# Kernel optimization log

Hardware: AMD Instinct MI355X
Metric: run time of the kernel (lower is better)

The kernel has to match this reference:

```python
import jax, jax.numpy as jnp
import numpy as np

K = 16
OP_LO, OP_HI = 0.05, 0.95
SC_LO, SC_HI = 0.01, 0.5
HIDDEN = 64
B, N_IN = 32, 8192
SAMPLE_RATIO = 0.1
JITTER_STD = 0.01
DENSITY_RADIUS = 0.1
EPS = 1e-6


def _naive_fps(points, m):
    # iterative farthest-point sampling, deterministic start at index 0
    Bb, Nn, _ = points.shape
    idx0 = jnp.zeros((Bb, m), jnp.int32)
    mind0 = jnp.full((Bb, Nn), 1e10, points.dtype)

    def body(i, carry):
        idx, mind = carry
        last = jnp.take_along_axis(points, idx[:, i - 1][:, None, None], axis=1)  # [B,1,3]
        d = jnp.sum((points - last) ** 2, axis=-1)  # [B,N]
        mind = jnp.minimum(mind, d)
        nxt = jnp.argmax(mind, axis=1).astype(jnp.int32)
        idx = idx.at[:, i].set(nxt)
        return idx, mind

    idx, _ = jax.lax.fori_loop(1, m, body, (idx0, mind0))
    return idx


def _axis_angle_to_R(aa):
    angle = jnp.linalg.norm(aa, axis=-1, keepdims=True)  # [B,N,1]
    axis = aa / (angle + EPS)
    x, y, z = axis[..., 0], axis[..., 1], axis[..., 2]
    a = angle[..., 0]
    ca, sa = jnp.cos(a), jnp.sin(a)
    C = 1.0 - ca
    row0 = jnp.stack([ca + x * x * C, x * y * C - z * sa, x * z * C + y * sa], axis=-1)
    row1 = jnp.stack([y * x * C + z * sa, ca + y * y * C, y * z * C - x * sa], axis=-1)
    row2 = jnp.stack([z * x * C - y * sa, z * y * C + x * sa, ca + z * z * C], axis=-1)
    return jnp.stack([row0, row1, row2], axis=-2)  # [B,N,3,3]


def _minmax_norm(v):
    lo = v.min(axis=1, keepdims=True)
    hi = v.max(axis=1, keepdims=True)
    return (v - lo) / (hi - lo + EPS)


def _forward(points, rw1, rb1, rw2, rb2, sw1, sb1, sw2, sb2):
    pts = points.astype(jnp.float32)
    Bb, Nn, _ = pts.shape
    m = int(Nn * SAMPLE_RATIO)
    idx = _naive_fps(jax.lax.stop_gradient(pts), m)
    sampled = jnp.take_along_axis(pts, jnp.broadcast_to(idx[:, :, None], (Bb, m, 3)), axis=1)
    noise = jax.random.normal(jax.random.key(42), sampled.shape, sampled.dtype) * JITTER_STD
    pts = jnp.concatenate([sampled, sampled + noise], axis=1)  # [B, 2m, 3]

    # kNN via squared distances (same ordering as torch.cdist euclidean)
    sq = jnp.sum(pts * pts, axis=-1)
    d2 = sq[:, :, None] + sq[:, None, :] - 2.0 * jnp.einsum('bnd,bmd->bnm', pts, pts)
    _, nn = jax.lax.top_k(-d2, K + 1)
    knn = nn[:, :, 1:]  # drop self, [B,N,K]
    neighbors = jax.vmap(lambda p, i: p[i])(pts, knn)  # [B,N,K,3]

    weighted_center = neighbors.mean(axis=2)  # [B,N,3]
    # rotation head: Linear -> GELU -> Linear
    h = jax.nn.gelu(weighted_center @ rw1 + rb1, approximate=False)
    axis_angle = h @ rw2 + rb2
    angle = jnp.linalg.norm(axis_angle, axis=-1, keepdims=True)
    too_small = angle < 1e-4
    safe_angle = jnp.where(too_small, 0.0, jnp.minimum(angle, 3.14))
    default_axis = jnp.array([1.0, 0.0, 0.0], jnp.float32)
    safe_axis = jnp.where(too_small, default_axis, axis_angle / (angle + EPS))
    R = _axis_angle_to_R(safe_axis * safe_angle)

    # scale head: Linear -> GELU -> Linear -> Softplus -> Hardtanh
    hs = jax.nn.gelu(pts @ sw1 + sb1, approximate=False)
    scale = jnp.clip(jax.nn.softplus(hs @ sw2 + sb2), SC_LO, SC_HI)

    # cov = R @ diag(scale^2) @ R^T
    cov = jnp.einsum('bnij,bnj,bnkj->bnik', R, scale * scale, R)

    # opacity from neighborhood covariance spectrum + local density
    centered = neighbors - pts[:, :, None, :]  # [B,N,K,3]
    ncov = jnp.einsum('bnki,bnkj->bnij', centered, centered) / (K - 1 + EPS)
    s = jnp.linalg.svd(ncov, compute_uv=False)  # descending singular values [B,N,3]
    linearness = s[..., 0] / (s[..., 1] + s[..., 2] + EPS)
    dist2 = jnp.sum(centered * centered, axis=-1)
    density = jnp.mean((dist2 < DENSITY_RADIUS ** 2).astype(jnp.float32), axis=2)
    combined = _minmax_norm(linearness) * _minmax_norm(density) ** 0.45
    opacity = jnp.clip(combined, OP_LO, OP_HI)

    return pts, cov, opacity, R, scale


def setup_inputs() -> dict:
    key = jax.random.key(0)
    ks = jax.random.split(key, 9)

    def lin(k, fan_in, shape):
        b = 1.0 / np.sqrt(fan_in)
        return jax.random.uniform(k, shape, jnp.float32, -b, b)

    return {
        'points': jax.random.normal(ks[0], (B, N_IN, 3), jnp.float32),
        'rw1': lin(ks[1], 3, (3, HIDDEN)), 'rb1': lin(ks[2], 3, (HIDDEN,)),
        'rw2': lin(ks[3], HIDDEN, (HIDDEN, 3)), 'rb2': lin(ks[4], HIDDEN, (3,)),
        'sw1': lin(ks[5], 3, (3, HIDDEN)), 'sb1': lin(ks[6], 3, (HIDDEN,)),
        'sw2': lin(ks[7], HIDDEN, (HIDDEN, 3)), 'sb2': lin(ks[8], HIDDEN, (3,)),
    }


def reference(points, rw1, rb1, rw2, rb2, sw1, sb1, sw2, sb2):
    return _forward(points, rw1, rb1, rw2, rb2, sw1, sb1, sw2, sb2)
```

## Files before the change

kernel.cpp:

```cpp
#include <hip/hip_runtime.h>
#include <math.h>

#define BB 32
#define N_IN 8192
#define M 819
#define M2 1638
#define KNN 16
#define RPB 64
#define NCH 4
#define CHLEN 410

__device__ __forceinline__ unsigned tf_rotl(unsigned x, int r){ return (x<<r)|(x>>(32-r)); }

__device__ __forceinline__ float erfinv_xla_f32(float x){
  float w = -log1pf(-__fmul_rn(x,x));
  float p;
  if (w < 5.0f) {
    w = __fsub_rn(w, 2.5f);
    p = 2.81022636e-08f;
    p = fmaf(p, w, 3.43273939e-07f);
    p = fmaf(p, w, -3.5233877e-06f);
    p = fmaf(p, w, -4.39150654e-06f);
    p = fmaf(p, w, 0.00021858087f);
    p = fmaf(p, w, -0.00125372503f);
    p = fmaf(p, w, -0.00417768164f);
    p = fmaf(p, w, 0.246640727f);
    p = fmaf(p, w, 1.50140941f);
  } else {
    w = __fsub_rn(sqrtf(w), 3.0f);
    p = -0.000200214257f;
    p = fmaf(p, w, 0.000100950558f);
    p = fmaf(p, w, 0.00134934322f);
    p = fmaf(p, w, -0.00367342844f);
    p = fmaf(p, w, 0.00573950773f);
    p = fmaf(p, w, -0.0076224613f);
    p = fmaf(p, w, 0.00943887047f);
    p = fmaf(p, w, 1.00167406f);
    p = fmaf(p, w, 2.83297682f);
  }
  return __fmul_rn(p, x);
}

__device__ __forceinline__ float noise_at(unsigned e){
  unsigned x0 = 0u, x1 = e;
  const unsigned k0 = 0u, k1 = 42u, k2 = 0u ^ 42u ^ 0x1BD11BDAu;
  x0 += k0; x1 += k1;
#define TFR(r) { x0 += x1; x1 = tf_rotl(x1, r); x1 ^= x0; }
  TFR(13) TFR(15) TFR(26) TFR(6)   x0 += k1; x1 += k2 + 1u;
  TFR(17) TFR(29) TFR(16) TFR(24)  x0 += k2; x1 += k0 + 2u;
  TFR(13) TFR(15) TFR(26) TFR(6)   x0 += k0; x1 += k1 + 3u;
  TFR(17) TFR(29) TFR(16) TFR(24)  x0 += k1; x1 += k2 + 4u;
  TFR(13) TFR(15) TFR(26) TFR(6)   x0 += k2; x1 += k0 + 5u;
#undef TFR
  unsigned bits = x0 ^ x1;
  float f = __uint_as_float((bits >> 9) | 0x3f800000u) - 1.0f;
  const float lo = -0.99999994f;
  float u = fmaf(f, 2.0f, lo);
  u = fmaxf(lo, u);
  float z = erfinv_xla_f32(u);
  float nrm = __fmul_rn(__uint_as_float(0x3FB504F3u), z);
  return __fmul_rn(nrm, 0.01f);
}

__device__ __forceinline__ unsigned long long dpp_max_u64(unsigned long long k, const int ctrl){
  int lo = (int)(unsigned)(k & 0xffffffffull);
  int hi = (int)(unsigned)(k >> 32);
  int slo, shi;
  switch (ctrl) {
    case 0x111: slo = __builtin_amdgcn_update_dpp(lo, lo, 0x111, 0xF, 0xF, false);
                shi = __builtin_amdgcn_update_dpp(hi, hi, 0x111, 0xF, 0xF, false); break;
    case 0x112: slo = __builtin_amdgcn_update_dpp(lo, lo, 0x112, 0xF, 0xF, false);
                shi = __builtin_amdgcn_update_dpp(hi, hi, 0x112, 0xF, 0xF, false); break;
    case 0x114: slo = __builtin_amdgcn_update_dpp(lo, lo, 0x114, 0xF, 0xF, false);
                shi = __builtin_amdgcn_update_dpp(hi, hi, 0x114, 0xF, 0xF, false); break;
    case 0x118: slo = __builtin_amdgcn_update_dpp(lo, lo, 0x118, 0xF, 0xF, false);
                shi = __builtin_amdgcn_update_dpp(hi, hi, 0x118, 0xF, 0xF, false); break;
    case 0x142: slo = __builtin_amdgcn_update_dpp(lo, lo, 0x142, 0xF, 0xF, false);
                shi = __builtin_amdgcn_update_dpp(hi, hi, 0x142, 0xF, 0xF, false); break;
    default:    slo = __builtin_amdgcn_update_dpp(lo, lo, 0x143, 0xF, 0xF, false);
                shi = __builtin_amdgcn_update_dpp(hi, hi, 0x143, 0xF, 0xF, false); break;
  }
  unsigned long long o = ((unsigned long long)(unsigned)shi << 32) | (unsigned)slo;
  return (o > k) ? o : k;
}

__global__ __launch_bounds__(256, 1) void fps_kernel(const float* __restrict__ pin,
                                                     float* __restrict__ ptsO){
  const int b = blockIdx.x;
  const int t = threadIdx.x;
  const float* P = pin + (size_t)b * N_IN * 3;

  __shared__ float s_x[N_IN], s_y[N_IN], s_z[N_IN];
  __shared__ int   s_sel[M];
  __shared__ unsigned s_klo[2][4], s_khi[2][4];

  for (int i = t; i < N_IN; i += 256) {
    s_x[i] = P[i*3+0]; s_y[i] = P[i*3+1]; s_z[i] = P[i*3+2];
  }
  float px[32], py[32], pz[32], mind[32];
#pragma unroll
  for (int k = 0; k < 32; ++k) {
    int p = t + (k<<8);
    px[k] = P[p*3+0]; py[k] = P[p*3+1]; pz[k] = P[p*3+2];
    mind[k] = 1e10f;
  }
  if (t == 0) s_sel[0] = 0;
  float lx = P[0], ly = P[1], lz = P[2];
  __syncthreads();

  for (int i = 1; i < M; ++i) {
    float bv = -1.0f; int bi = 0x7fffffff;
#pragma unroll
    for (int k = 0; k < 32; ++k) {
      float dx = __fsub_rn(px[k], lx);
      float dy = __fsub_rn(py[k], ly);
      float dz = __fsub_rn(pz[k], lz);
      float d  = __fadd_rn(__fadd_rn(__fmul_rn(dx,dx), __fmul_rn(dy,dy)), __fmul_rn(dz,dz));
      float m  = fminf(mind[k], d);
      mind[k] = m;
      int idx  = t + (k<<8);
      if (m > bv) { bv = m; bi = idx; }
    }
    unsigned long long key = ((unsigned long long)__float_as_uint(bv) << 32) | (unsigned)(~bi);
    key = dpp_max_u64(key, 0x111);
    key = dpp_max_u64(key, 0x112);
    key = dpp_max_u64(key, 0x114);
    key = dpp_max_u64(key, 0x118);
    key = dpp_max_u64(key, 0x142);
    key = dpp_max_u64(key, 0x143);
    unsigned klo = (unsigned)__builtin_amdgcn_readlane((int)(unsigned)(key & 0xffffffffull), 63);
    unsigned khi = (unsigned)__builtin_amdgcn_readlane((int)(unsigned)(key >> 32), 63);
    int par = i & 1;
    if ((t & 63) == 0) { s_klo[par][t>>6] = klo; s_khi[par][t>>6] = khi; }
    __syncthreads();
    unsigned long long kb = ((unsigned long long)s_khi[par][0] << 32) | s_klo[par][0];
#pragma unroll
    for (int w2 = 1; w2 < 4; ++w2) {
      unsigned long long ko = ((unsigned long long)s_khi[par][w2] << 32) | s_klo[par][w2];
      if (ko > kb) kb = ko;
    }
    int bsel = (int)(~(unsigned)(kb & 0xffffffffull));
    if (t == 0) s_sel[i] = bsel;
    lx = s_x[bsel]; ly = s_y[bsel]; lz = s_z[bsel];
  }
  __syncthreads();

  for (int j = t; j < M; j += 256) {
    int sj = s_sel[j];
    float x = s_x[sj], y = s_y[sj], z = s_z[sj];
    float* o0 = ptsO + ((size_t)b*M2 + j)*3;
    float* o1 = o0 + (size_t)M*3;
    o0[0]=x; o0[1]=y; o0[2]=z;
    unsigned e0 = (unsigned)(b*M + j) * 3u;
    o1[0] = __fadd_rn(x, noise_at(e0+0u));
    o1[1] = __fadd_rn(y, noise_at(e0+1u));
    o1[2] = __fadd_rn(z, noise_at(e0+2u));
  }
}

__device__ __forceinline__ float gelu_f(float x){
  return x * (erff(x / 1.41421356237f) + 1.0f) * 0.5f;
}
__device__ __forceinline__ float softplus_f(float x){
  return fmaxf(x, 0.0f) + log1pf(expf(-fabsf(x)));
}
__device__ __forceinline__ void eig3_sym(double a00,double a01,double a02,double a11,double a12,double a22,
                                         double& s0o, double& s1o, double& s2o){
  double p1 = a01*a01 + a02*a02 + a12*a12;
  double q  = (a00+a11+a22)/3.0;
  double b00=a00-q, b11=a11-q, b22=a22-q;
  double p2 = b00*b00+b11*b11+b22*b22 + 2.0*p1;
  double e0,e1,e2;
  if (p2 <= 0.0) { e0=e1=e2=q; }
  else {
    double p  = sqrt(p2/6.0);
    double ip = 1.0/p;
    double c00=b00*ip, c01=a01*ip, c02=a02*ip, c11=b11*ip, c12=a12*ip, c22=b22*ip;
    double detB = c00*(c11*c22-c12*c12) - c01*(c01*c22-c12*c02) + c02*(c01*c12-c11*c02);
    double r = 0.5*detB;
    r = fmin(1.0, fmax(-1.0, r));
    double phi = acos(r)/3.0;
    e0 = q + 2.0*p*cos(phi);
    e2 = q + 2.0*p*cos(phi + 2.0943951023931953);
    e1 = 3.0*q - e0 - e2;
  }
  double s0 = fabs(e0), s1 = fabs(e1), s2 = fabs(e2), t;
  if (s0 < s1){t=s0;s0=s1;s1=t;}
  if (s1 < s2){t=s1;s1=s2;s2=t;}
  if (s0 < s1){t=s0;s0=s1;s1=t;}
  s0o=s0; s1o=s1; s2o=s2;
}

__device__ __forceinline__ void ins17(float d2, int j, float bd[17], int bix[17]){
  bool c[17];
#pragma unroll
  for (int k = 0; k < 17; ++k) c[k] = d2 < bd[k];
#pragma unroll
  for (int k = 16; k > 0; --k) {
    bd[k]  = c[k-1] ? bd[k-1] : (c[k] ? d2 : bd[k]);
    bix[k] = c[k-1] ? bix[k-1] : (c[k] ? j : bix[k]);
  }
  if (c[0]) { bd[0] = d2; bix[0] = j; }
}

__device__ __forceinline__ unsigned fmono(float f){
  unsigned u = __float_as_uint(f);
  return (u & 0x80000000u) ? ~u : (u | 0x80000000u);
}

__global__ __launch_bounds__(256) void knn_select(const float* __restrict__ ptsG,
                                                  float* __restrict__ RO){
  const int b = blockIdx.x, tid = threadIdx.x;

  __shared__ __align__(16) unsigned char smem[28416];
  float4* sp = (float4*)smem;

  for (int i = tid; i < M2; i += 256) {
    const float* p = ptsG + ((size_t)b*M2 + i)*3;
    float x=p[0], y=p[1], z=p[2];
    float sq = __fadd_rn(__fadd_rn(__fmul_rn(x,x),__fmul_rn(y,y)),__fmul_rn(z,z));
    sp[i] = make_float4(x,y,z,sq);
  }
  __syncthreads();

  const int rl    = tid >> 2;
  const int chunk = tid & 3;
  const int row   = blockIdx.y*RPB + rl;
  const bool valid = row < M2;

  float4 me = sp[valid ? row : 0];
  const float px = me.x, py = me.y, pz = me.z, psq = me.w;

  float bd[17]; int bix[17];
#pragma unroll
  for (int k=0;k<17;++k){ bd[k]=3.4e38f; bix[k]=0x7fffffff; }

  const int j0 = chunk*CHLEN;
  const int j1 = (j0 + CHLEN < M2) ? (j0 + CHLEN) : M2;
  for (int j = j0; j < j1; j += 2) {
    float4 qa = sp[j];
    float4 qb = sp[j+1];
    float dota = fmaf(pz, qa.z, fmaf(py, qa.y, __fmul_rn(px, qa.x)));
    float d2a  = __fsub_rn(__fadd_rn(psq, qa.w), __fmul_rn(2.0f, dota));
    float dotb = fmaf(pz, qb.z, fmaf(py, qb.y, __fmul_rn(px, qb.x)));
    float d2b  = __fsub_rn(__fadd_rn(psq, qb.w), __fmul_rn(2.0f, dotb));
    if (fminf(d2a, d2b) < bd[16]) {
      if (d2a < bd[16]) ins17(d2a, j,   bd, bix);
      if (d2b < bd[16]) ins17(d2b, j+1, bd, bix);
    }
  }
  __syncthreads();

  unsigned*       s_key = (unsigned*)smem;
  unsigned short* s_idx = (unsigned short*)(smem + 17408);
  unsigned short* s_nbr = (unsigned short*)(smem + 26112);

  if (valid) {
    const int basel = (rl*NCH + chunk)*17;
#pragma unroll
    for (int k = 0; k < 17; ++k) {
      s_key[basel + k] = fmono(bd[k]);
      s_idx[basel + k] = (unsigned short)bix[k];
    }
  }
  __syncthreads();

  if (chunk == 0 && valid) {
    int h0=0, h1=0, h2=0, h3=0;
    const int lb = rl*NCH*17;
    for (int e = 0; e < 17; ++e) {
      unsigned k0 = s_key[lb      + h0]; int i0 = s_idx[lb      + h0];
      unsigned k1 = s_key[lb + 17 + h1]; int i1 = s_idx[lb + 17 + h1];
      unsigned k2 = s_key[lb + 34 + h2]; int i2 = s_idx[lb + 34 + h2];
      unsigned k3 = s_key[lb + 51 + h3]; int i3 = s_idx[lb + 51 + h3];
      unsigned bk = k0; int bj = i0; int bc = 0;
      if (k1 < bk || (k1 == bk && i1 < bj)) { bk = k1; bj = i1; bc = 1; }
      if (k2 < bk || (k2 == bk && i2 < bj)) { bk = k2; bj = i2; bc = 2; }
      if (k3 < bk || (k3 == bk && i3 < bj)) { bk = k3; bj = i3; bc = 3; }
      h0 += (bc == 0); h1 += (bc == 1); h2 += (bc == 2); h3 += (bc == 3);
      if (e > 0) s_nbr[rl*16 + (e-1)] = (unsigned short)bj;
    }
    uint* kout = (uint*)(RO + ((size_t)b*M2 + row)*9);
#pragma unroll
    for (int k = 0; k < 8; ++k)
      kout[k] = (uint)s_nbr[rl*16 + 2*k] | ((uint)s_nbr[rl*16 + 2*k + 1] << 16);
  }
}

__global__ __launch_bounds__(256) void geom_kernel(
    const float* __restrict__ ptsG,
    const float* __restrict__ rw1, const float* __restrict__ rb1,
    const float* __restrict__ rw2, const float* __restrict__ rb2,
    const float* __restrict__ sw1, const float* __restrict__ sb1,
    const float* __restrict__ sw2, const float* __restrict__ sb2,
    float* __restrict__ covO, float* __restrict__ RO, float* __restrict__ scO,
    float* __restrict__ linW, float* __restrict__ denW)
{
  const int tid = threadIdx.x;
  __shared__ float w_rw1[192], w_rb1[64], w_rw2[192], w_rb2[3];
  __shared__ float w_sw1[192], w_sb1[64], w_sw2[192], w_sb2[3];
  if (tid < 192) { w_rw1[tid]=rw1[tid]; w_rw2[tid]=rw2[tid]; w_sw1[tid]=sw1[tid]; w_sw2[tid]=sw2[tid]; }
  if (tid < 64) { w_rb1[tid]=rb1[tid]; w_sb1[tid]=sb1[tid]; }
  if (tid < 3)  { w_rb2[tid]=rb2[tid]; w_sb2[tid]=sb2[tid]; }
  __syncthreads();

  const int gid = blockIdx.x*256 + tid;
  if (gid >= BB*M2) return;
  const int b = gid / M2;
  const size_t base = (size_t)gid;

  const uint* kin = (const uint*)(RO + base*9);
  uint kw[8];
#pragma unroll
  for (int k = 0; k < 8; ++k) kw[k] = kin[k];
  asm volatile("" ::: "memory");

  int nidx[16];
#pragma unroll
  for (int k = 0; k < 8; ++k) { nidx[2*k] = (int)(kw[k] & 0xffffu); nidx[2*k+1] = (int)(kw[k] >> 16); }

  const float* meP = ptsG + base*3;
  const float px = meP[0], py = meP[1], pz = meP[2];
  const double pxd = (double)px, pyd = (double)py, pzd = (double)pz;

  float nx[16], ny[16], nz[16];
#pragma unroll
  for (int k = 0; k < 16; ++k) {
    const float* np = ptsG + ((size_t)b*M2 + nidx[k])*3;
    nx[k] = np[0]; ny[k] = np[1]; nz[k] = np[2];
  }

  float wcx=0.f, wcy=0.f, wcz=0.f;
#pragma unroll
  for (int k=0;k<16;++k){ wcx += nx[k]; wcy += ny[k]; wcz += nz[k]; }
  wcx *= 0.0625f; wcy *= 0.0625f; wcz *= 0.0625f;

  float aa0=0.f, aa1=0.f, aa2=0.f;
  for (int j = 0; j < 64; ++j) {
    float hp = __fadd_rn(__fadd_rn(__fadd_rn(__fmul_rn(wcx,w_rw1[j]), __fmul_rn(wcy,w_rw1[64+j])),
                                   __fmul_rn(wcz,w_rw1[128+j])), w_rb1[j]);
    float h = gelu_f(hp);
    aa0 += h*w_rw2[j*3+0]; aa1 += h*w_rw2[j*3+1]; aa2 += h*w_rw2[j*3+2];
  }
  aa0 += w_rb2[0]; aa1 += w_rb2[1]; aa2 += w_rb2[2];

  float angle = sqrtf(__fadd_rn(__fadd_rn(__fmul_rn(aa0,aa0),__fmul_rn(aa1,aa1)),__fmul_rn(aa2,aa2)));
  bool  tsml  = angle < 1e-4f;
  float sang  = tsml ? 0.0f : fminf(angle, 3.14f);
  float ax, ay, az;
  if (tsml) { ax=1.0f; ay=0.0f; az=0.0f; }
  else { float inv = angle + 1e-6f; ax = aa0/inv; ay = aa1/inv; az = aa2/inv; }

  float v0 = ax*sang, v1 = ay*sang, v2 = az*sang;
  float ang2 = sqrtf(__fadd_rn(__fadd_rn(__fmul_rn(v0,v0),__fmul_rn(v1,v1)),__fmul_rn(v2,v2)));
  float inv2 = ang2 + 1e-6f;
  float x = v0/inv2, y = v1/inv2, z = v2/inv2;
  float ca = cosf(ang2), sa = sinf(ang2), Cc = 1.0f - ca;
  float R00 = ca + x*x*Cc,   R01 = x*y*Cc - z*sa, R02 = x*z*Cc + y*sa;
  float R10 = y*x*Cc + z*sa, R11 = ca + y*y*Cc,   R12 = y*z*Cc - x*sa;
  float R20 = z*x*Cc - y*sa, R21 = z*y*Cc + x*sa, R22 = ca + z*z*Cc;

  float sp0=0.f, sp1=0.f, sp2=0.f;
  for (int j = 0; j < 64; ++j) {
    float hp = __fadd_rn(__fadd_rn(__fadd_rn(__fmul_rn(px,w_sw1[j]), __fmul_rn(py,w_sw1[64+j])),
                                   __fmul_rn(pz,w_sw1[128+j])), w_sb1[j]);
    float h = gelu_f(hp);
    sp0 += h*w_sw2[j*3+0]; sp1 += h*w_sw2[j*3+1]; sp2 += h*w_sw2[j*3+2];
  }
  sp0 += w_sb2[0]; sp1 += w_sb2[1]; sp2 += w_sb2[2];
  float sc0 = fminf(fmaxf(softplus_f(sp0), 0.01f), 0.5f);
  float sc1 = fminf(fmaxf(softplus_f(sp1), 0.01f), 0.5f);
  float sc2 = fminf(fmaxf(softplus_f(sp2), 0.01f), 0.5f);

  float s2x = sc0*sc0, s2y = sc1*sc1, s2z = sc2*sc2;
  float T00 = R00*s2x, T01 = R01*s2y, T02 = R02*s2z;
  float T10 = R10*s2x, T11 = R11*s2y, T12 = R12*s2z;
  float T20 = R20*s2x, T21 = R21*s2y, T22 = R22*s2z;
  float C00 = T00*R00 + T01*R01 + T02*R02;
  float C01 = T00*R10 + T01*R11 + T02*R12;
  float C02 = T00*R20 + T01*R21 + T02*R22;
  float C10 = T10*R00 + T11*R01 + T12*R02;
  float C11 = T10*R10 + T11*R11 + T12*R12;
  float C12 = T10*R20 + T11*R21 + T12*R22;
  float C20 = T20*R00 + T21*R01 + T22*R02;
  float C21 = T20*R10 + T21*R11 + T22*R12;
  float C22 = T20*R20 + T21*R21 + T22*R22;

  double n00=0.,n01=0.,n02=0.,n11=0.,n12=0.,n22=0.;
  int cnt = 0;
  const double R2 = 0.1*0.1;
#pragma unroll
  for (int k=0;k<16;++k){
    double cx = (double)nx[k] - pxd;
    double cy = (double)ny[k] - pyd;
    double cz = (double)nz[k] - pzd;
    n00 += cx*cx; n01 += cx*cy; n02 += cx*cz;
    n11 += cy*cy; n12 += cy*cz; n22 += cz*cz;
    double dd = cx*cx + cy*cy + cz*cz;
    if (dd < R2) cnt++;
  }
  const double inv15 = 15.0 + 1e-6;
  n00/=inv15; n01/=inv15; n02/=inv15; n11/=inv15; n12/=inv15; n22/=inv15;

  double sv0, sv1, sv2;
  eig3_sym(n00,n01,n02,n11,n12,n22, sv0, sv1, sv2);
  float lin = (float)(sv0 / (sv1 + sv2 + 1e-6));
  float den = (float)cnt / 16.0f;

  float* cO = covO + base*9;
  cO[0]=C00; cO[1]=C01; cO[2]=C02; cO[3]=C10; cO[4]=C11; cO[5]=C12; cO[6]=C20; cO[7]=C21; cO[8]=C22;
  float* rO = RO + base*9;
  rO[0]=R00; rO[1]=R01; rO[2]=R02; rO[3]=R10; rO[4]=R11; rO[5]=R12; rO[6]=R20; rO[7]=R21; rO[8]=R22;
  float* sO = scO + base*3;
  sO[0]=sc0; sO[1]=sc1; sO[2]=sc2;
  linW[base] = lin;
  denW[base] = den;
}

__global__ __launch_bounds__(256) void minmax_k(const float* __restrict__ linW,
                                                const float* __restrict__ denW,
                                                float* __restrict__ mmW){
  const int b = blockIdx.x, t = threadIdx.x;
  float lmin=3.4e38f, lmax=-3.4e38f, dmin=3.4e38f, dmax=-3.4e38f;
  for (int i = t; i < M2; i += 256) {
    float l = linW[b*M2+i], d = denW[b*M2+i];
    lmin=fminf(lmin,l); lmax=fmaxf(lmax,l);
    dmin=fminf(dmin,d); dmax=fmaxf(dmax,d);
  }
#pragma unroll
  for (int off = 32; off > 0; off >>= 1) {
    lmin=fminf(lmin,__shfl_down(lmin,(unsigned)off));
    lmax=fmaxf(lmax,__shfl_down(lmax,(unsigned)off));
    dmin=fminf(dmin,__shfl_down(dmin,(unsigned)off));
    dmax=fmaxf(dmax,__shfl_down(dmax,(unsigned)off));
  }
  __shared__ float s[4][4];
  int w = t >> 6;
  if ((t & 63) == 0) { s[w][0]=lmin; s[w][1]=lmax; s[w][2]=dmin; s[w][3]=dmax; }
  __syncthreads();
  if (t == 0) {
    for (int i = 1; i < 4; ++i) {
      s[0][0]=fminf(s[0][0],s[i][0]); s[0][1]=fmaxf(s[0][1],s[i][1]);
      s[0][2]=fminf(s[0][2],s[i][2]); s[0][3]=fmaxf(s[0][3],s[i][3]);
    }
    mmW[b*4+0]=s[0][0]; mmW[b*4+1]=s[0][1]; mmW[b*4+2]=s[0][2]; mmW[b*4+3]=s[0][3];
  }
}

__global__ void opacity_k(const float* __restrict__ linW, const float* __restrict__ denW,
                          const float* __restrict__ mmW, float* __restrict__ opO){
  int gid = blockIdx.x*blockDim.x + threadIdx.x;
  if (gid >= BB*M2) return;
  int b = gid / M2;
  float lmin=mmW[b*4+0], lmax=mmW[b*4+1], dmin=mmW[b*4+2], dmax=mmW[b*4+3];
  float nl = (linW[gid]-lmin) / ((lmax-lmin) + 1e-6f);
  float nd = (denW[gid]-dmin) / ((dmax-dmin) + 1e-6f);
  float comb = nl * powf(nd, 0.45f);
  opO[gid] = fminf(fmaxf(comb, 0.05f), 0.95f);
}

extern "C" void kernel_launch(void* const* d_in, const int* in_sizes, int n_in,
                              void* d_out, int out_size, void* d_ws, size_t ws_size,
                              hipStream_t stream) {
  const float* pin = (const float*)d_in[0];
  const float* rw1 = (const float*)d_in[1];
  const float* rb1 = (const float*)d_in[2];
  const float* rw2 = (const float*)d_in[3];
  const float* rb2 = (const float*)d_in[4];
  const float* sw1 = (const float*)d_in[5];
  const float* sb1 = (const float*)d_in[6];
  const float* sw2 = (const float*)d_in[7];
  const float* sb2 = (const float*)d_in[8];

  float* out  = (float*)d_out;
  float* ptsO = out;
  float* covO = ptsO + (size_t)BB*M2*3;
  float* opO  = covO + (size_t)BB*M2*9;
  float* RO   = opO  + (size_t)BB*M2;
  float* scO  = RO   + (size_t)BB*M2*9;

  float* linW = (float*)d_ws + (size_t)BB*M;
  float* denW = linW + (size_t)BB*M2;
  float* mmW  = denW + (size_t)BB*M2;

  fps_kernel<<<BB, 256, 0, stream>>>(pin, ptsO);
  dim3 g2(BB, (M2 + RPB - 1)/RPB);
  knn_select<<<g2, 256, 0, stream>>>(ptsO, RO);
  geom_kernel<<<(BB*M2 + 255)/256, 256, 0, stream>>>(ptsO, rw1, rb1, rw2, rb2, sw1, sb1, sw2, sb2,
                                                     covO, RO, scO, linW, denW);
  minmax_k<<<BB, 256, 0, stream>>>(linW, denW, mmW);
  opacity_k<<<(BB*M2 + 255)/256, 256, 0, stream>>>(linW, denW, mmW, opO);
}
```

Measured before the change: 1.294 ms.

## Widen FPS blocks to 512 threads and split kNN rows into eight chunks

The farthest-point-sampling kernel now runs 512 threads per batch, so each thread holds 16 points instead of 32 and the cross-wave reduction reads eight wave candidates written by lane 63 instead of using readlane. The kNN kernel processes 32 rows per block with 8 chunks per row, and packs key and index into one 64-bit value to simplify the 8-way merge. The intent is to shorten the serial per-iteration work in FPS, which dominates since only 32 blocks run, and to raise kNN parallelism. In exchange, FPS pays for a larger block barrier on each of its 819 iterations, and the kNN merge step does more work per row in a single thread.

```diff
diff --git a/kernel.cpp b/kernel.cpp
--- a/kernel.cpp
+++ b/kernel.cpp
@@ -6,9 +6,9 @@
 #define M 819
 #define M2 1638
 #define KNN 16
-#define RPB 64
-#define NCH 4
-#define CHLEN 410
+#define RPB 32
+#define NCH 8
+#define CHLEN 206
 
 __device__ __forceinline__ unsigned tf_rotl(unsigned x, int r){ return (x<<r)|(x>>(32-r)); }
 
@@ -84,7 +84,7 @@
   return (o > k) ? o : k;
 }
 
-__global__ __launch_bounds__(256, 1) void fps_kernel(const float* __restrict__ pin,
+__global__ __launch_bounds__(512, 1) void fps_kernel(const float* __restrict__ pin,
                                                      float* __restrict__ ptsO){
   const int b = blockIdx.x;
   const int t = threadIdx.x;
@@ -92,15 +92,15 @@
 
   __shared__ float s_x[N_IN], s_y[N_IN], s_z[N_IN];
   __shared__ int   s_sel[M];
-  __shared__ unsigned s_klo[2][4], s_khi[2][4];
-
-  for (int i = t; i < N_IN; i += 256) {
+  __shared__ unsigned s_cand[2][8][2];
+
+  for (int i = t; i < N_IN; i += 512) {
     s_x[i] = P[i*3+0]; s_y[i] = P[i*3+1]; s_z[i] = P[i*3+2];
   }
-  float px[32], py[32], pz[32], mind[32];
-#pragma unroll
-  for (int k = 0; k < 32; ++k) {
-    int p = t + (k<<8);
+  float px[16], py[16], pz[16], mind[16];
+#pragma unroll
+  for (int k = 0; k < 16; ++k) {
+    int p = t + (k<<9);
     px[k] = P[p*3+0]; py[k] = P[p*3+1]; pz[k] = P[p*3+2];
     mind[k] = 1e10f;
   }
@@ -111,14 +111,14 @@
   for (int i = 1; i < M; ++i) {
     float bv = -1.0f; int bi = 0x7fffffff;
 #pragma unroll
-    for (int k = 0; k < 32; ++k) {
+    for (int k = 0; k < 16; ++k) {
       float dx = __fsub_rn(px[k], lx);
       float dy = __fsub_rn(py[k], ly);
       float dz = __fsub_rn(pz[k], lz);
       float d  = __fadd_rn(__fadd_rn(__fmul_rn(dx,dx), __fmul_rn(dy,dy)), __fmul_rn(dz,dz));
       float m  = fminf(mind[k], d);
       mind[k] = m;
-      int idx  = t + (k<<8);
+      int idx  = t + (k<<9);
       if (m > bv) { bv = m; bi = idx; }
     }
     unsigned long long key = ((unsigned long long)__float_as_uint(bv) << 32) | (unsigned)(~bi);
@@ -128,15 +128,16 @@
     key = dpp_max_u64(key, 0x118);
     key = dpp_max_u64(key, 0x142);
     key = dpp_max_u64(key, 0x143);
-    unsigned klo = (unsigned)__builtin_amdgcn_readlane((int)(unsigned)(key & 0xffffffffull), 63);
-    unsigned khi = (unsigned)__builtin_amdgcn_readlane((int)(unsigned)(key >> 32), 63);
     int par = i & 1;
-    if ((t & 63) == 0) { s_klo[par][t>>6] = klo; s_khi[par][t>>6] = khi; }
+    if ((t & 63) == 63) {
+      s_cand[par][t>>6][0] = (unsigned)(key & 0xffffffffull);
+      s_cand[par][t>>6][1] = (unsigned)(key >> 32);
+    }
     __syncthreads();
-    unsigned long long kb = ((unsigned long long)s_khi[par][0] << 32) | s_klo[par][0];
-#pragma unroll
-    for (int w2 = 1; w2 < 4; ++w2) {
-      unsigned long long ko = ((unsigned long long)s_khi[par][w2] << 32) | s_klo[par][w2];
+    unsigned long long kb = ((unsigned long long)s_cand[par][0][1] << 32) | s_cand[par][0][0];
+#pragma unroll
+    for (int w2 = 1; w2 < 8; ++w2) {
+      unsigned long long ko = ((unsigned long long)s_cand[par][w2][1] << 32) | s_cand[par][w2][0];
       if (ko > kb) kb = ko;
     }
     int bsel = (int)(~(unsigned)(kb & 0xffffffffull));
@@ -145,7 +146,7 @@
   }
   __syncthreads();
 
-  for (int j = t; j < M; j += 256) {
+  for (int j = t; j < M; j += 512) {
     int sj = s_sel[j];
     float x = s_x[sj], y = s_y[sj], z = s_z[sj];
     float* o0 = ptsO + ((size_t)b*M2 + j)*3;
@@ -212,7 +213,7 @@
                                                   float* __restrict__ RO){
   const int b = blockIdx.x, tid = threadIdx.x;
 
-  __shared__ __align__(16) unsigned char smem[28416];
+  __shared__ __align__(16) unsigned char smem[35840];
   float4* sp = (float4*)smem;
 
   for (int i = tid; i < M2; i += 256) {
@@ -223,8 +224,8 @@
   }
   __syncthreads();
 
-  const int rl    = tid >> 2;
-  const int chunk = tid & 3;
+  const int rl    = tid >> 3;
+  const int chunk = tid & 7;
   const int row   = blockIdx.y*RPB + rl;
   const bool valid = row < M2;
 
@@ -251,34 +252,40 @@
   }
   __syncthreads();
 
-  unsigned*       s_key = (unsigned*)smem;
-  unsigned short* s_idx = (unsigned short*)(smem + 17408);
-  unsigned short* s_nbr = (unsigned short*)(smem + 26112);
+  unsigned long long* s_kid = (unsigned long long*)smem;
+  unsigned short*     s_nbr = (unsigned short*)(smem + 34816);
 
   if (valid) {
     const int basel = (rl*NCH + chunk)*17;
 #pragma unroll
-    for (int k = 0; k < 17; ++k) {
-      s_key[basel + k] = fmono(bd[k]);
-      s_idx[basel + k] = (unsigned short)bix[k];
-    }
+    for (int k = 0; k < 17; ++k)
+      s_kid[basel + k] = ((unsigned long long)fmono(bd[k]) << 32) | (unsigned)bix[k];
   }
   __syncthreads();
 
   if (chunk == 0 && valid) {
-    int h0=0, h1=0, h2=0, h3=0;
+    int h0=0,h1=0,h2=0,h3=0,h4=0,h5=0,h6=0,h7=0;
     const int lb = rl*NCH*17;
     for (int e = 0; e < 17; ++e) {
-      unsigned k0 = s_key[lb      + h0]; int i0 = s_idx[lb      + h0];
-      unsigned k1 = s_key[lb + 17 + h1]; int i1 = s_idx[lb + 17 + h1];
-      unsigned k2 = s_key[lb + 34 + h2]; int i2 = s_idx[lb + 34 + h2];
-      unsigned k3 = s_key[lb + 51 + h3]; int i3 = s_idx[lb + 51 + h3];
-      unsigned bk = k0; int bj = i0; int bc = 0;
-      if (k1 < bk || (k1 == bk && i1 < bj)) { bk = k1; bj = i1; bc = 1; }
-      if (k2 < bk || (k2 == bk && i2 < bj)) { bk = k2; bj = i2; bc = 2; }
-      if (k3 < bk || (k3 == bk && i3 < bj)) { bk = k3; bj = i3; bc = 3; }
-      h0 += (bc == 0); h1 += (bc == 1); h2 += (bc == 2); h3 += (bc == 3);
-      if (e > 0) s_nbr[rl*16 + (e-1)] = (unsigned short)bj;
+      unsigned long long k0 = s_kid[lb        + h0];
+      unsigned long long k1 = s_kid[lb + 17   + h1];
+      unsigned long long k2 = s_kid[lb + 34   + h2];
+      unsigned long long k3 = s_kid[lb + 51   + h3];
+      unsigned long long k4 = s_kid[lb + 68   + h4];
+      unsigned long long k5 = s_kid[lb + 85   + h5];
+      unsigned long long k6 = s_kid[lb + 102  + h6];
+      unsigned long long k7 = s_kid[lb + 119  + h7];
+      unsigned long long bk = k0; int bc = 0;
+      if (k1 < bk) { bk = k1; bc = 1; }
+      if (k2 < bk) { bk = k2; bc = 2; }
+      if (k3 < bk) { bk = k3; bc = 3; }
+      if (k4 < bk) { bk = k4; bc = 4; }
+      if (k5 < bk) { bk = k5; bc = 5; }
+      if (k6 < bk) { bk = k6; bc = 6; }
+      if (k7 < bk) { bk = k7; bc = 7; }
+      h0 += (bc==0); h1 += (bc==1); h2 += (bc==2); h3 += (bc==3);
+      h4 += (bc==4); h5 += (bc==5); h6 += (bc==6); h7 += (bc==7);
+      if (e > 0) s_nbr[rl*16 + (e-1)] = (unsigned short)(bk & 0xffffu);
     }
     uint* kout = (uint*)(RO + ((size_t)b*M2 + row)*9);
 #pragma unroll
@@ -483,7 +490,7 @@
   float* denW = linW + (size_t)BB*M2;
   float* mmW  = denW + (size_t)BB*M2;
 
-  fps_kernel<<<BB, 256, 0, stream>>>(pin, ptsO);
+  fps_kernel<<<BB, 512, 0, stream>>>(pin, ptsO);
   dim3 g2(BB, (M2 + RPB - 1)/RPB);
   knn_select<<<g2, 256, 0, stream>>>(ptsO, RO);
   geom_kernel<<<(BB*M2 + 255)/256, 256, 0, stream>>>(ptsO, rw1, rb1, rw2, rb2, sw1, sb1, sw2, sb2,
```

Result: faster. 1.204 ms (median of 2 runs) (-7.0%).
